# Performance work log

Hardware: AMD Instinct MI355X
Metric: run time of the kernel (lower is better)

## Reference

```python
import jax, jax.numpy as jnp
import numpy as np

B, S, D_MODEL, D_K, D_V = 8, 2048, 1024, 64, 64
NEG = -1e9


def setup_inputs() -> dict:
    key = jax.random.key(0)
    ks = jax.random.split(key, 12)
    inv = 1.0 / np.sqrt(D_MODEL)
    return {
        "q": jax.random.normal(ks[0], (B, S, D_MODEL), jnp.float32),
        "k": jax.random.normal(ks[1], (B, S, D_MODEL), jnp.float32),
        "v": jax.random.normal(ks[2], (B, S, D_MODEL), jnp.float32),
        "mask": jax.random.randint(ks[3], (1, S, S), 0, 2, jnp.int32),
        # Linear weights stored as [in, out] so y = x @ W + b
        "Wq": jax.random.normal(ks[4], (D_MODEL, D_K), jnp.float32) * inv,
        "bq": jnp.zeros((D_K,), jnp.float32),
        "Wk": jax.random.normal(ks[5], (D_MODEL, D_K), jnp.float32) * inv,
        "bk": jnp.zeros((D_K,), jnp.float32),
        "Wv": jax.random.normal(ks[6], (D_MODEL, D_V), jnp.float32) * inv,
        "bv": jnp.zeros((D_V,), jnp.float32),
        "Wo": jax.random.normal(ks[7], (D_V, D_MODEL), jnp.float32) * (1.0 / np.sqrt(D_V)),
        "bo": jnp.zeros((D_MODEL,), jnp.float32),
    }


def reference(q, k, v, mask, Wq, bq, Wk, bk, Wv, bv, Wo, bo):
    # single-head projections: [b, s, d_model] -> [b, s, d_k/d_v]
    qp = q @ Wq + bq
    kp = k @ Wk + bk
    vp = v @ Wv + bv
    # UNSCALED dot-product scores (original has no 1/sqrt(d_k)): [b, s, s]
    scores = jnp.einsum("bqd,bkd->bqk", qp, kp)
    scores = jnp.where(mask == 0, jnp.float32(NEG), scores)
    attn = jax.nn.softmax(scores, axis=-1)  # dropout p=0.0 -> identity
    out = jnp.einsum("bqk,bkv->bqv", attn, vp)
    return out @ Wo + bo
```

## Files before the change

kernel.cpp:

```cpp
#include <hip/hip_runtime.h>
#include <hip/hip_bf16.h>

typedef __bf16 bf16_t;
typedef __attribute__((ext_vector_type(8))) __bf16 bf16x8;
typedef __attribute__((ext_vector_type(4))) float f32x4;

#define MFMA16(a, b, c) __builtin_amdgcn_mfma_f32_16x16x32_bf16((a), (b), (c), 0, 0, 0)

#define NB 8
#define SS 2048
#define DM 1024
#define DK 64
#define NROW (NB * SS)
#define NSPLIT 4
#define SPLEN (SS / NSPLIT)

typedef __attribute__((address_space(1))) const unsigned int ga_u32;
typedef __attribute__((address_space(3))) unsigned int ls_u32;
#define GLOAD16(g, l) \
  __builtin_amdgcn_global_load_lds((ga_u32*)(g), (ls_u32*)(l), 16, 0, 0)

union U16x8 { unsigned short u[8]; uint4 q; };
union U16x4 { unsigned short u[4]; ushort4 v; };

__device__ inline void split_hl(float x, unsigned short& h, unsigned short& l) {
  bf16_t hb = (bf16_t)x;
  bf16_t lb = (bf16_t)(x - (float)hb);
  h = *(unsigned short*)&hb;
  l = *(unsigned short*)&lb;
}

__global__ __launch_bounds__(256) void maskpack_kernel(
    const int* __restrict__ mask, unsigned int* __restrict__ mbits) {
  int idx = blockIdx.x * 256 + threadIdx.x;
  int q = idx >> 6, w = idx & 63;
  const int4* src = (const int4*)(mask + (q << 11) + (w << 5));
  unsigned int bits = 0u;
#pragma unroll
  for (int i = 0; i < 8; ++i) {
    int4 t = src[i];
    bits |= (t.x != 0 ? 1u : 0u) << (i * 4 + 0);
    bits |= (t.y != 0 ? 1u : 0u) << (i * 4 + 1);
    bits |= (t.z != 0 ? 1u : 0u) << (i * 4 + 2);
    bits |= (t.w != 0 ? 1u : 0u) << (i * 4 + 3);
  }
  mbits[idx] = bits;
}

__global__ __launch_bounds__(256) void wprep_kernel(
    const float* __restrict__ Wq, const float* __restrict__ Wk,
    const float* __restrict__ Wv, char* __restrict__ wimg) {
  int which = blockIdx.x >> 6;
  const float* W = which == 0 ? Wq : (which == 1 ? Wk : Wv);
  char* img = wimg + (size_t)which * 16 * 16384;
  int e = (blockIdx.x & 63) * 256 + threadIdx.x;
  int k = e >> 4, n0 = (e & 15) << 2;
  float4 f = *(const float4*)(W + k * 64 + n0);
  float fv[4] = {f.x, f.y, f.z, f.w};
  char* base = img + (k >> 6) * 16384;
  int kk = k & 63;
#pragma unroll
  for (int u = 0; u < 4; ++u) {
    int n = n0 + u;
    unsigned short h, l;
    split_hl(fv[u], h, l);
    int byte = n * 128 + ((2 * kk) ^ ((n & 7) << 4));
    *(unsigned short*)(base + byte) = h;
    *(unsigned short*)(base + 8192 + byte) = l;
  }
}

__global__ __launch_bounds__(256) void proj3_kernel(
    const float* __restrict__ qx, const float* __restrict__ kx,
    const float* __restrict__ vx, const char* __restrict__ wimg,
    const float* __restrict__ bq, const float* __restrict__ bk,
    const float* __restrict__ bv, bf16_t* __restrict__ qhi,
    bf16_t* __restrict__ qlo, char* __restrict__ kimg,
    char* __restrict__ vimg) {
  __shared__ __align__(16) char smem[32768];
  char* xbuf = smem;
  char* wbuf = smem + 16384;
  const int mode = blockIdx.y;
  const float* X = mode == 0 ? qx : (mode == 1 ? kx : vx);
  const float* bias = mode == 0 ? bq : (mode == 1 ? bk : bv);
  const int tid = threadIdx.x;
  const int lane = tid & 63;
  const int wv = tid >> 6;
  const int lr = lane & 15;
  const int g = lane >> 4;
  const int rbase = blockIdx.x * 64;
  const int xr = tid >> 2;
  const int kg = (tid & 3) << 4;
  const int row_local = wv * 16 + lr;
  const int swa = (row_local & 7) << 4;
  const int swx = (xr & 7) << 4;

  f32x4 acc[4] = {};
  const char* wsrc0 = wimg + (size_t)mode * 16 * 16384;

  for (int ch = 0; ch < 16; ++ch) {
    __syncthreads();
    const char* wsrc = wsrc0 + ch * 16384;
#pragma unroll
    for (int u = 0; u < 4; ++u)
      GLOAD16(wsrc + u * 4096 + tid * 16, wbuf + u * 4096 + tid * 16);
    {
      const float4* xp =
          (const float4*)(X + (size_t)(rbase + xr) * DM + ch * 64 + kg);
      float4 a = xp[0], b4 = xp[1], c4 = xp[2], d4 = xp[3];
      float xv[16] = {a.x,  a.y,  a.z,  a.w,  b4.x, b4.y, b4.z, b4.w,
                      c4.x, c4.y, c4.z, c4.w, d4.x, d4.y, d4.z, d4.w};
      U16x8 hq[2], lq[2];
#pragma unroll
      for (int i = 0; i < 16; ++i)
        split_hl(xv[i], hq[i >> 3].u[i & 7], lq[i >> 3].u[i & 7]);
      char* xh = xbuf + xr * 128;
      int b0 = 2 * kg;
      *(uint4*)(xh + ((b0) ^ swx)) = hq[0].q;
      *(uint4*)(xh + ((b0 + 16) ^ swx)) = hq[1].q;
      *(uint4*)(xh + 8192 + ((b0) ^ swx)) = lq[0].q;
      *(uint4*)(xh + 8192 + ((b0 + 16) ^ swx)) = lq[1].q;
    }
    asm volatile("s_waitcnt vmcnt(0)\n" ::: "memory");
    __syncthreads();
#pragma unroll
    for (int ks = 0; ks < 2; ++ks) {
      int co = ks * 64 + g * 16;
      bf16x8 ah = *(const bf16x8*)(xbuf + row_local * 128 + (co ^ swa));
      bf16x8 al = *(const bf16x8*)(xbuf + 8192 + row_local * 128 + (co ^ swa));
#pragma unroll
      for (int c = 0; c < 4; ++c) {
        int n = c * 16 + lr;
        int swb = (n & 7) << 4;
        bf16x8 bh = *(const bf16x8*)(wbuf + n * 128 + (co ^ swb));
        bf16x8 bl = *(const bf16x8*)(wbuf + 8192 + n * 128 + (co ^ swb));
        acc[c] = MFMA16(ah, bl, acc[c]);
        acc[c] = MFMA16(al, bh, acc[c]);
        acc[c] = MFMA16(ah, bh, acc[c]);
      }
    }
  }
  __syncthreads();
  float* sacc = (float*)smem;
#pragma unroll
  for (int c = 0; c < 4; ++c)
#pragma unroll
    for (int j = 0; j < 4; ++j)
      sacc[(wv * 16 + g * 4 + j) * 69 + c * 16 + lr] = acc[c][j];
  __syncthreads();

  const int b = rbase >> 11;
  const int t = (rbase & (SS - 1)) >> 6;
  if (mode == 0) {
    int r = tid & 63, cg = tid >> 6;
    int row = rbase + r;
    U16x8 h0, h1, l0, l1;
#pragma unroll
    for (int i = 0; i < 16; ++i) {
      float v = sacc[r * 69 + cg * 16 + i] + bias[cg * 16 + i];
      if (i < 8) split_hl(v, h0.u[i & 7], l0.u[i & 7]);
      else       split_hl(v, h1.u[i & 7], l1.u[i & 7]);
    }
    *(uint4*)((char*)qhi + (size_t)row * 128 + cg * 32) = h0.q;
    *(uint4*)((char*)qhi + (size_t)row * 128 + cg * 32 + 16) = h1.q;
    *(uint4*)((char*)qlo + (size_t)row * 128 + cg * 32) = l0.q;
    *(uint4*)((char*)qlo + (size_t)row * 128 + cg * 32 + 16) = l1.q;
  } else if (mode == 1) {
    int r = tid & 63, cg = tid >> 6;
    char* base = kimg + (((size_t)(b * 32 + t)) << 14);
    int sw = (r & 7) << 4;
#pragma unroll
    for (int m = 0; m < 4; ++m) {
      U16x4 hv, lv;
#pragma unroll
      for (int u = 0; u < 4; ++u) {
        int col = cg * 16 + m * 4 + u;
        float v = sacc[r * 69 + col] + bias[col];
        split_hl(v, hv.u[u], lv.u[u]);
      }
      int off = (cg * 32 + m * 8) ^ sw;
      *(ushort4*)(base + r * 128 + off) = hv.v;
      *(ushort4*)(base + 8192 + r * 128 + off) = lv.v;
    }
  } else {
    int d = tid & 63, rg = tid >> 6;
    char* base = vimg + (((size_t)(b * 32 + t)) << 14);
    int sw = (d & 7) << 4;
    float bv = bias[d];
#pragma unroll
    for (int m = 0; m < 4; ++m) {
      U16x4 hv, lv;
#pragma unroll
      for (int u = 0; u < 4; ++u) {
        int r = rg * 16 + m * 4 + u;
        float v = sacc[r * 69 + d] + bv;
        split_hl(v, hv.u[u], lv.u[u]);
      }
      int off = (rg * 32 + m * 8) ^ sw;
      *(ushort4*)(base + d * 128 + off) = hv.v;
      *(ushort4*)(base + 8192 + d * 128 + off) = lv.v;
    }
  }
}

__global__ __launch_bounds__(256) void attn_kernel(
    const bf16_t* __restrict__ qhi, const bf16_t* __restrict__ qlo,
    const char* __restrict__ kimg, const char* __restrict__ vimg,
    const unsigned int* __restrict__ mbits, float* __restrict__ part_acc,
    float* __restrict__ part_m, float* __restrict__ part_l) {
  __shared__ __align__(16) char kbuf[16384];
  __shared__ __align__(16) char vbuf[16384];
  __shared__ __align__(16) char plds_all[4][2048];
  const int tid = threadIdx.x;
  const int lane = tid & 63;
  const int wv = tid >> 6;
  const int lr = lane & 15;
  const int g = lane >> 4;
  char* plds = &plds_all[wv][0];
  const int qrow0 = (blockIdx.x * 4 + wv) * 16;
  const int split = blockIdx.y;
  const int kv0 = split * SPLEN;
  const int b = qrow0 >> 11;
  const int sq0 = (qrow0 & (SS - 1)) + g * 4;

  const bf16_t* qh = qhi + (qrow0 + lr) * DK + g * 8;
  const bf16_t* ql = qlo + (qrow0 + lr) * DK + g * 8;
  bf16x8 qh0 = *(const bf16x8*)qh;
  bf16x8 qh1 = *(const bf16x8*)(qh + 32);
  bf16x8 ql0 = *(const bf16x8*)ql;
  bf16x8 ql1 = *(const bf16x8*)(ql + 32);

  float m[4], lsum[4];
  f32x4 acc[4] = {};
#pragma unroll
  for (int j = 0; j < 4; ++j) { m[j] = -3.0e38f; lsum[j] = 0.f; }

  for (int it = 0; it < SPLEN / 64; ++it) {
    const int tglob = (kv0 >> 6) + it;
    const char* ksrc = kimg + (((size_t)(b * 32 + tglob)) << 14);
    const char* vsrc = vimg + (((size_t)(b * 32 + tglob)) << 14);
#pragma unroll
    for (int u = 0; u < 4; ++u) {
      GLOAD16(ksrc + tid * 16 + u * 4096, kbuf + tid * 16 + u * 4096);
      GLOAD16(vsrc + tid * 16 + u * 4096, vbuf + tid * 16 + u * 4096);
    }
    asm volatile("s_waitcnt vmcnt(0)\n" ::: "memory");
    __syncthreads();
    f32x4 sac[4];
#pragma unroll
    for (int t = 0; t < 4; ++t) {
      int rk = t * 16 + lr;
      int sw = (rk & 7) << 4;
      bf16x8 kh0 = *(const bf16x8*)(kbuf + rk * 128 + ((g * 16) ^ sw));
      bf16x8 kh1 = *(const bf16x8*)(kbuf + rk * 128 + ((64 + g * 16) ^ sw));
      bf16x8 kl0 = *(const bf16x8*)(kbuf + 8192 + rk * 128 + ((g * 16) ^ sw));
      bf16x8 kl1 =
          *(const bf16x8*)(kbuf + 8192 + rk * 128 + ((64 + g * 16) ^ sw));
      f32x4 s = {};
      s = MFMA16(qh0, kl0, s);
      s = MFMA16(qh1, kl1, s);
      s = MFMA16(ql0, kh0, s);
      s = MFMA16(ql1, kh1, s);
      s = MFMA16(qh0, kh0, s);
      s = MFMA16(qh1, kh1, s);
      sac[t] = s;
    }
    const int wbase = (kv0 >> 5) + it * 2;
    uint2 m2[4];
#pragma unroll
    for (int j = 0; j < 4; ++j)
      m2[j] = *(const uint2*)(mbits + (sq0 + j) * 64 + wbase);
#pragma unroll
    for (int t = 0; t < 4; ++t)
#pragma unroll
      for (int j = 0; j < 4; ++j) {
        unsigned w = (t & 2) ? m2[j].y : m2[j].x;
        if (!((w >> ((t & 1) * 16 + lr)) & 1u)) sac[t][j] = -1e9f;
      }
#pragma unroll
    for (int j = 0; j < 4; ++j) {
      float v = sac[0][j];
#pragma unroll
      for (int t = 1; t < 4; ++t) v = fmaxf(v, sac[t][j]);
      v = fmaxf(v, __shfl_xor(v, 1, 64));
      v = fmaxf(v, __shfl_xor(v, 2, 64));
      v = fmaxf(v, __shfl_xor(v, 4, 64));
      v = fmaxf(v, __shfl_xor(v, 8, 64));
      float mn = fmaxf(m[j], v);
      float sc = __expf(m[j] - mn);
      m[j] = mn;
      lsum[j] *= sc;
#pragma unroll
      for (int c = 0; c < 4; ++c) acc[c][j] *= sc;
    }
    float ps[4] = {0.f, 0.f, 0.f, 0.f};
#pragma unroll
    for (int t = 0; t < 4; ++t)
#pragma unroll
      for (int j = 0; j < 4; ++j) {
        float p = __expf(sac[t][j] - m[j]);
        bf16_t pb = (bf16_t)p;
        ps[j] += (float)pb;
        int row = g * 4 + j;
        int byte = row * 128 + (((t * 16 + lr) * 2) ^ ((row & 7) << 4));
        *(bf16_t*)(plds + byte) = pb;
      }
#pragma unroll
    for (int j = 0; j < 4; ++j) {
      float s_ = ps[j];
      s_ += __shfl_xor(s_, 1, 64);
      s_ += __shfl_xor(s_, 2, 64);
      s_ += __shfl_xor(s_, 4, 64);
      s_ += __shfl_xor(s_, 8, 64);
      lsum[j] += s_;
    }
    asm volatile("s_waitcnt lgkmcnt(0)\n" ::: "memory");
#pragma unroll
    for (int kt = 0; kt < 2; ++kt) {
      int pbyte = lr * 128 + ((kt * 64 + g * 16) ^ ((lr & 7) << 4));
      bf16x8 pa = *(const bf16x8*)(plds + pbyte);
#pragma unroll
      for (int c = 0; c < 4; ++c) {
        int n = c * 16 + lr;
        int swv = (n & 7) << 4;
        bf16x8 vfh = *(const bf16x8*)(vbuf + n * 128 + ((kt * 64 + g * 16) ^ swv));
        bf16x8 vfl =
            *(const bf16x8*)(vbuf + 8192 + n * 128 + ((kt * 64 + g * 16) ^ swv));
        acc[c] = MFMA16(pa, vfh, acc[c]);
        acc[c] = MFMA16(pa, vfl, acc[c]);
      }
    }
    __syncthreads();
  }
#pragma unroll
  for (int c = 0; c < 4; ++c)
#pragma unroll
    for (int j = 0; j < 4; ++j)
      part_acc[((size_t)split * NROW + qrow0 + g * 4 + j) * DK + c * 16 + lr] =
          acc[c][j];
  if (lr == 0) {
#pragma unroll
    for (int j = 0; j < 4; ++j) {
      part_m[split * NROW + qrow0 + g * 4 + j] = m[j];
      part_l[split * NROW + qrow0 + g * 4 + j] = lsum[j];
    }
  }
}

__global__ __launch_bounds__(256) void combine_kernel(
    const float* __restrict__ pacc, const float* __restrict__ pm,
    const float* __restrict__ pl, float* __restrict__ attn_f) {
  int idx = blockIdx.x * 256 + threadIdx.x;
  int row = idx >> 6;
  float m0 = pm[row], m1 = pm[NROW + row];
  float m2 = pm[2 * NROW + row], m3 = pm[3 * NROW + row];
  float M = fmaxf(fmaxf(m0, m1), fmaxf(m2, m3));
  float w0 = __expf(m0 - M), w1 = __expf(m1 - M);
  float w2 = __expf(m2 - M), w3 = __expf(m3 - M);
  float l = w0 * pl[row] + w1 * pl[NROW + row] + w2 * pl[2 * NROW + row] +
            w3 * pl[3 * NROW + row];
  float a = w0 * pacc[idx] + w1 * pacc[(size_t)NROW * DK + idx] +
            w2 * pacc[2 * (size_t)NROW * DK + idx] +
            w3 * pacc[3 * (size_t)NROW * DK + idx];
  attn_f[idx] = a / l;
}

__global__ __launch_bounds__(256) void oproj_kernel(
    const float* __restrict__ attn, const float* __restrict__ Wo,
    const float* __restrict__ bo, float* __restrict__ out) {
  __shared__ __align__(16) bf16_t wt[256 * 64];
  const int tid = threadIdx.x;
  const int lane = tid & 63;
  const int wv = tid >> 6;
  const int lr = lane & 15;
  const int g = lane >> 4;
  const int rbase = blockIdx.x * 64 + wv * 16;
  const int c0 = blockIdx.y * 256;
  {
    const int k = tid >> 2;
    const int n0 = (tid & 3) << 6;
    const float4* src = (const float4*)(Wo + k * DM + c0 + n0);
#pragma unroll
    for (int i = 0; i < 16; ++i) {
      float4 f = src[i];
      float fv[4] = {f.x, f.y, f.z, f.w};
#pragma unroll
      for (int u = 0; u < 4; ++u) {
        int n = n0 + i * 4 + u;
        int byte = (n << 7) + (k << 1);
        byte ^= (n & 7) << 4;
        *(bf16_t*)((char*)wt + byte) = (bf16_t)fv[u];
      }
    }
  }
  __syncthreads();
  const float* ab = attn + (rbase + lr) * DK + g * 8;
  float4 x0 = *(const float4*)ab;
  float4 x1 = *(const float4*)(ab + 4);
  float4 y0 = *(const float4*)(ab + 32);
  float4 y1 = *(const float4*)(ab + 36);
  float xv[8] = {x0.x, x0.y, x0.z, x0.w, x1.x, x1.y, x1.z, x1.w};
  float yv[8] = {y0.x, y0.y, y0.z, y0.w, y1.x, y1.y, y1.z, y1.w};
  bf16x8 ah0, al0, ah1, al1;
#pragma unroll
  for (int i = 0; i < 8; ++i) {
    ah0[i] = (bf16_t)xv[i];
    al0[i] = (bf16_t)(xv[i] - (float)ah0[i]);
    ah1[i] = (bf16_t)yv[i];
    al1[i] = (bf16_t)(yv[i] - (float)ah1[i]);
  }
  f32x4 acc[16] = {};
#pragma unroll
  for (int c = 0; c < 16; ++c) {
    int n = c * 16 + lr;
    int byte0 = (n << 7) + ((g * 8) << 1);
    byte0 ^= (n & 7) << 4;
    int byte1 = (n << 7) + ((32 + g * 8) << 1);
    byte1 ^= (n & 7) << 4;
    bf16x8 b0 = *(const bf16x8*)((const char*)wt + byte0);
    bf16x8 b1 = *(const bf16x8*)((const char*)wt + byte1);
    acc[c] = MFMA16(ah0, b0, acc[c]);
    acc[c] = MFMA16(al0, b0, acc[c]);
    acc[c] = MFMA16(ah1, b1, acc[c]);
    acc[c] = MFMA16(al1, b1, acc[c]);
  }
#pragma unroll
  for (int c = 0; c < 16; ++c) {
    float bv = bo[c0 + c * 16 + lr];
#pragma unroll
    for (int j = 0; j < 4; ++j)
      out[(rbase + g * 4 + j) * DM + c0 + c * 16 + lr] = acc[c][j] + bv;
  }
}

extern "C" void kernel_launch(void* const* d_in, const int* in_sizes, int n_in,
                              void* d_out, int out_size, void* d_ws,
                              size_t ws_size, hipStream_t stream) {
  const float* q = (const float*)d_in[0];
  const float* k = (const float*)d_in[1];
  const float* v = (const float*)d_in[2];
  const int* mask = (const int*)d_in[3];
  const float* Wq = (const float*)d_in[4];
  const float* bq = (const float*)d_in[5];
  const float* Wk = (const float*)d_in[6];
  const float* bk = (const float*)d_in[7];
  const float* Wv = (const float*)d_in[8];
  const float* bv = (const float*)d_in[9];
  const float* Wo = (const float*)d_in[10];
  const float* bo = (const float*)d_in[11];
  float* out = (float*)d_out;

  bf16_t* qhi = (bf16_t*)d_ws;
  bf16_t* qlo = qhi + (size_t)NROW * DK;
  char* kimg = (char*)(qlo + (size_t)NROW * DK);
  char* vimg = kimg + ((size_t)NB * 32 << 14);
  char* wimg = vimg + ((size_t)NB * 32 << 14);
  float* part_acc = (float*)(wimg + (size_t)3 * 16 * 16384);
  float* part_m = part_acc + (size_t)NSPLIT * NROW * DK;
  float* part_l = part_m + (size_t)NSPLIT * NROW;
  float* attn_f = part_l + (size_t)NSPLIT * NROW;
  unsigned int* mbits = (unsigned int*)(attn_f + (size_t)NROW * DK);

  maskpack_kernel<<<dim3(SS * (SS / 32) / 256), dim3(256), 0, stream>>>(mask,
                                                                        mbits);
  wprep_kernel<<<dim3(192), dim3(256), 0, stream>>>(Wq, Wk, Wv, wimg);
  proj3_kernel<<<dim3(NROW / 64, 3), dim3(256), 0, stream>>>(
      q, k, v, wimg, bq, bk, bv, qhi, qlo, kimg, vimg);
  attn_kernel<<<dim3(NROW / 64, NSPLIT), dim3(256), 0, stream>>>(
      qhi, qlo, kimg, vimg, mbits, part_acc, part_m, part_l);
  combine_kernel<<<dim3(NROW * DK / 256), dim3(256), 0, stream>>>(
      part_acc, part_m, part_l, attn_f);
  oproj_kernel<<<dim3(NROW / 64, DM / 256), dim3(256), 0, stream>>>(attn_f, Wo,
                                                                    bo, out);
}
```

Measured before the change: 142.3 us.

## Double-buffer weight tiles and prefetch X registers in projection kernel

Reworks the projection kernel's K-loop into a software pipeline. Weight chunks are staged into two alternating LDS buffers via global_load_lds, and the X input for two chunks ahead is prefetched into registers, using explicit vmcnt/lgkmcnt waits and barriers. The aim is to overlap global memory latency with the MFMA compute that the previous loop serialized. It increases LDS use from 32KB to 48KB, which can lower occupancy, and the hand-counted waitcnts are fragile.

```diff
diff --git a/kernel.cpp b/kernel.cpp
--- a/kernel.cpp
+++ b/kernel.cpp
@@ -77,9 +77,8 @@
     const float* __restrict__ bv, bf16_t* __restrict__ qhi,
     bf16_t* __restrict__ qlo, char* __restrict__ kimg,
     char* __restrict__ vimg) {
-  __shared__ __align__(16) char smem[32768];
+  __shared__ __align__(16) char smem[49152];
   char* xbuf = smem;
-  char* wbuf = smem + 16384;
   const int mode = blockIdx.y;
   const float* X = mode == 0 ? qx : (mode == 1 ? kx : vx);
   const float* bias = mode == 0 ? bq : (mode == 1 ? bk : bv);
@@ -98,31 +97,33 @@
   f32x4 acc[4] = {};
   const char* wsrc0 = wimg + (size_t)mode * 16 * 16384;
 
-  for (int ch = 0; ch < 16; ++ch) {
-    __syncthreads();
+  float4 xa, xb, xc, xd;
+  auto issueX = [&](int ch) {
+    const float4* xp =
+        (const float4*)(X + (size_t)(rbase + xr) * DM + ch * 64 + kg);
+    xa = xp[0]; xb = xp[1]; xc = xp[2]; xd = xp[3];
+  };
+  auto writeX = [&]() {
+    float xv[16] = {xa.x, xa.y, xa.z, xa.w, xb.x, xb.y, xb.z, xb.w,
+                    xc.x, xc.y, xc.z, xc.w, xd.x, xd.y, xd.z, xd.w};
+    U16x8 hq[2], lq[2];
+#pragma unroll
+    for (int i = 0; i < 16; ++i)
+      split_hl(xv[i], hq[i >> 3].u[i & 7], lq[i >> 3].u[i & 7]);
+    char* xh = xbuf + xr * 128;
+    int b0 = 2 * kg;
+    *(uint4*)(xh + (b0 ^ swx)) = hq[0].q;
+    *(uint4*)(xh + ((b0 + 16) ^ swx)) = hq[1].q;
+    *(uint4*)(xh + 8192 + (b0 ^ swx)) = lq[0].q;
+    *(uint4*)(xh + 8192 + ((b0 + 16) ^ swx)) = lq[1].q;
+  };
+  auto stageW = [&](int ch, char* dst) {
     const char* wsrc = wsrc0 + ch * 16384;
 #pragma unroll
     for (int u = 0; u < 4; ++u)
-      GLOAD16(wsrc + u * 4096 + tid * 16, wbuf + u * 4096 + tid * 16);
-    {
-      const float4* xp =
-          (const float4*)(X + (size_t)(rbase + xr) * DM + ch * 64 + kg);
-      float4 a = xp[0], b4 = xp[1], c4 = xp[2], d4 = xp[3];
-      float xv[16] = {a.x,  a.y,  a.z,  a.w,  b4.x, b4.y, b4.z, b4.w,
-                      c4.x, c4.y, c4.z, c4.w, d4.x, d4.y, d4.z, d4.w};
-      U16x8 hq[2], lq[2];
-#pragma unroll
-      for (int i = 0; i < 16; ++i)
-        split_hl(xv[i], hq[i >> 3].u[i & 7], lq[i >> 3].u[i & 7]);
-      char* xh = xbuf + xr * 128;
-      int b0 = 2 * kg;
-      *(uint4*)(xh + ((b0) ^ swx)) = hq[0].q;
-      *(uint4*)(xh + ((b0 + 16) ^ swx)) = hq[1].q;
-      *(uint4*)(xh + 8192 + ((b0) ^ swx)) = lq[0].q;
-      *(uint4*)(xh + 8192 + ((b0 + 16) ^ swx)) = lq[1].q;
-    }
-    asm volatile("s_waitcnt vmcnt(0)\n" ::: "memory");
-    __syncthreads();
+      GLOAD16(wsrc + u * 4096 + tid * 16, dst + u * 4096 + tid * 16);
+  };
+  auto compute = [&](const char* wb) {
 #pragma unroll
     for (int ks = 0; ks < 2; ++ks) {
       int co = ks * 64 + g * 16;
@@ -132,12 +133,43 @@
       for (int c = 0; c < 4; ++c) {
         int n = c * 16 + lr;
         int swb = (n & 7) << 4;
-        bf16x8 bh = *(const bf16x8*)(wbuf + n * 128 + (co ^ swb));
-        bf16x8 bl = *(const bf16x8*)(wbuf + 8192 + n * 128 + (co ^ swb));
+        bf16x8 bh = *(const bf16x8*)(wb + n * 128 + (co ^ swb));
+        bf16x8 bl = *(const bf16x8*)(wb + 8192 + n * 128 + (co ^ swb));
         acc[c] = MFMA16(ah, bl, acc[c]);
         acc[c] = MFMA16(al, bh, acc[c]);
         acc[c] = MFMA16(ah, bh, acc[c]);
       }
+    }
+  };
+
+  issueX(0);
+  stageW(0, smem + 16384);
+  writeX();
+  issueX(1);
+  asm volatile("s_waitcnt vmcnt(4)" ::: "memory");
+  asm volatile("s_waitcnt lgkmcnt(0)" ::: "memory");
+  __builtin_amdgcn_s_barrier();
+  __builtin_amdgcn_sched_barrier(0);
+
+  for (int ch = 0; ch < 16; ++ch) {
+    char* wc = (ch & 1) ? smem + 32768 : smem + 16384;
+    char* wn = (ch & 1) ? smem + 16384 : smem + 32768;
+    if (ch < 15) stageW(ch + 1, wn);
+    compute(wc);
+    if (ch < 15) {
+      __builtin_amdgcn_sched_barrier(0);
+      __builtin_amdgcn_s_barrier();
+      __builtin_amdgcn_sched_barrier(0);
+      writeX();
+      if (ch < 14) {
+        issueX(ch + 2);
+        asm volatile("s_waitcnt vmcnt(4)" ::: "memory");
+      } else {
+        asm volatile("s_waitcnt vmcnt(0)" ::: "memory");
+      }
+      asm volatile("s_waitcnt lgkmcnt(0)" ::: "memory");
+      __builtin_amdgcn_s_barrier();
+      __builtin_amdgcn_sched_barrier(0);
     }
   }
   __syncthreads();
```

New measurement: 140.6 us (median of 3 runs). Within noise of the previous version (-1.2%).

## Restructure QKV projection: 32-row tiles, async fp32 X staging to LDS

Applied to the files above, without the earlier changes.

The projection kernel now processes 32 rows per block with a 2x2 wave tiling. Raw fp32 X rows are staged into LDS with async global-to-LDS loads in 256-column chunks. The hi/lo bf16 split is done per wave when the fragments are read, instead of through register loads and a split before the LDS store. The grid doubles and the output epilogues write 16-byte vectors. The intent is to make X loads asynchronous and raise parallelism. The cost is more LDS per block (about 49 KB), which may limit occupancy, and split work that is repeated across the wn waves.

```diff
diff --git a/kernel.cpp b/kernel.cpp
--- a/kernel.cpp
+++ b/kernel.cpp
@@ -77,129 +77,136 @@
     const float* __restrict__ bv, bf16_t* __restrict__ qhi,
     bf16_t* __restrict__ qlo, char* __restrict__ kimg,
     char* __restrict__ vimg) {
-  __shared__ __align__(16) char smem[32768];
+  __shared__ __align__(16) char smem[49664];
   char* xbuf = smem;
-  char* wbuf = smem + 16384;
+  char* wbuf = smem + 33280;
   const int mode = blockIdx.y;
   const float* X = mode == 0 ? qx : (mode == 1 ? kx : vx);
   const float* bias = mode == 0 ? bq : (mode == 1 ? bk : bv);
+  const char* Xb = (const char*)X;
   const int tid = threadIdx.x;
   const int lane = tid & 63;
   const int wv = tid >> 6;
   const int lr = lane & 15;
   const int g = lane >> 4;
-  const int rbase = blockIdx.x * 64;
-  const int xr = tid >> 2;
-  const int kg = (tid & 3) << 4;
-  const int row_local = wv * 16 + lr;
-  const int swa = (row_local & 7) << 4;
-  const int swx = (xr & 7) << 4;
-
-  f32x4 acc[4] = {};
+  const int wm = wv & 1;
+  const int wn = wv >> 1;
+  const int rbase = blockIdx.x * 32;
   const char* wsrc0 = wimg + (size_t)mode * 16 * 16384;
 
-  for (int ch = 0; ch < 16; ++ch) {
-    __syncthreads();
-    const char* wsrc = wsrc0 + ch * 16384;
-#pragma unroll
-    for (int u = 0; u < 4; ++u)
-      GLOAD16(wsrc + u * 4096 + tid * 16, wbuf + u * 4096 + tid * 16);
+  f32x4 acc[2] = {};
+
+  auto stageX = [&](int sc) {
+#pragma unroll
+    for (int j = 0; j < 8; ++j) {
+      int u = wv * 8 + j;
+      GLOAD16(Xb + (size_t)(rbase + u) * 4096 + sc * 1024 + lane * 16,
+              xbuf + u * 1040 + lane * 16);
+    }
+  };
+  auto stageW = [&](int idx) {
+    const char* wsrc = wsrc0 + idx * 16384;
+#pragma unroll
+    for (int v = 0; v < 4; ++v)
+      GLOAD16(wsrc + v * 4096 + tid * 16, wbuf + v * 4096 + tid * 16);
+  };
+
+  stageX(0);
+  stageW(0);
+  asm volatile("s_waitcnt vmcnt(0)" ::: "memory");
+  __builtin_amdgcn_s_barrier();
+  __builtin_amdgcn_sched_barrier(0);
+
+  for (int idx = 0; idx < 16; ++idx) {
     {
-      const float4* xp =
-          (const float4*)(X + (size_t)(rbase + xr) * DM + ch * 64 + kg);
-      float4 a = xp[0], b4 = xp[1], c4 = xp[2], d4 = xp[3];
-      float xv[16] = {a.x,  a.y,  a.z,  a.w,  b4.x, b4.y, b4.z, b4.w,
-                      c4.x, c4.y, c4.z, c4.w, d4.x, d4.y, d4.z, d4.w};
-      U16x8 hq[2], lq[2];
-#pragma unroll
-      for (int i = 0; i < 16; ++i)
-        split_hl(xv[i], hq[i >> 3].u[i & 7], lq[i >> 3].u[i & 7]);
-      char* xh = xbuf + xr * 128;
-      int b0 = 2 * kg;
-      *(uint4*)(xh + ((b0) ^ swx)) = hq[0].q;
-      *(uint4*)(xh + ((b0 + 16) ^ swx)) = hq[1].q;
-      *(uint4*)(xh + 8192 + ((b0) ^ swx)) = lq[0].q;
-      *(uint4*)(xh + 8192 + ((b0 + 16) ^ swx)) = lq[1].q;
-    }
-    asm volatile("s_waitcnt vmcnt(0)\n" ::: "memory");
-    __syncthreads();
-#pragma unroll
-    for (int ks = 0; ks < 2; ++ks) {
-      int co = ks * 64 + g * 16;
-      bf16x8 ah = *(const bf16x8*)(xbuf + row_local * 128 + (co ^ swa));
-      bf16x8 al = *(const bf16x8*)(xbuf + 8192 + row_local * 128 + (co ^ swa));
-#pragma unroll
-      for (int c = 0; c < 4; ++c) {
-        int n = c * 16 + lr;
-        int swb = (n & 7) << 4;
-        bf16x8 bh = *(const bf16x8*)(wbuf + n * 128 + (co ^ swb));
-        bf16x8 bl = *(const bf16x8*)(wbuf + 8192 + n * 128 + (co ^ swb));
-        acc[c] = MFMA16(ah, bl, acc[c]);
-        acc[c] = MFMA16(al, bh, acc[c]);
-        acc[c] = MFMA16(ah, bh, acc[c]);
+      const int sub = idx & 3;
+      const char* xrow = xbuf + (wm * 16 + lr) * 1040 + sub * 256;
+#pragma unroll
+      for (int ks = 0; ks < 2; ++ks) {
+        float4 f0 = *(const float4*)(xrow + ks * 128 + g * 32);
+        float4 f1 = *(const float4*)(xrow + ks * 128 + g * 32 + 16);
+        float xv[8] = {f0.x, f0.y, f0.z, f0.w, f1.x, f1.y, f1.z, f1.w};
+        bf16x8 ah, al;
+#pragma unroll
+        for (int i = 0; i < 8; ++i) {
+          unsigned short h, l;
+          split_hl(xv[i], h, l);
+          ((unsigned short*)&ah)[i] = h;
+          ((unsigned short*)&al)[i] = l;
+        }
+#pragma unroll
+        for (int c = 0; c < 2; ++c) {
+          int n = wn * 32 + c * 16 + lr;
+          int swb = (n & 7) << 4;
+          int co = ks * 64 + g * 16;
+          bf16x8 bh = *(const bf16x8*)(wbuf + n * 128 + (co ^ swb));
+          bf16x8 bl = *(const bf16x8*)(wbuf + 8192 + n * 128 + (co ^ swb));
+          acc[c] = MFMA16(ah, bl, acc[c]);
+          acc[c] = MFMA16(al, bh, acc[c]);
+          acc[c] = MFMA16(ah, bh, acc[c]);
+        }
       }
     }
-  }
+    __builtin_amdgcn_sched_barrier(0);
+    __builtin_amdgcn_s_barrier();
+    if (idx < 15) {
+      if ((idx & 3) == 3) stageX((idx >> 2) + 1);
+      stageW(idx + 1);
+      asm volatile("s_waitcnt vmcnt(0)" ::: "memory");
+      __builtin_amdgcn_s_barrier();
+      __builtin_amdgcn_sched_barrier(0);
+    }
+  }
+
   __syncthreads();
   float* sacc = (float*)smem;
 #pragma unroll
-  for (int c = 0; c < 4; ++c)
+  for (int c = 0; c < 2; ++c)
 #pragma unroll
     for (int j = 0; j < 4; ++j)
-      sacc[(wv * 16 + g * 4 + j) * 69 + c * 16 + lr] = acc[c][j];
+      sacc[(wm * 16 + g * 4 + j) * 69 + wn * 32 + c * 16 + lr] = acc[c][j];
   __syncthreads();
 
   const int b = rbase >> 11;
   const int t = (rbase & (SS - 1)) >> 6;
+  const int rt0 = rbase & 63;
   if (mode == 0) {
-    int r = tid & 63, cg = tid >> 6;
+    int r = tid & 31, cg = tid >> 5;
     int row = rbase + r;
-    U16x8 h0, h1, l0, l1;
-#pragma unroll
-    for (int i = 0; i < 16; ++i) {
-      float v = sacc[r * 69 + cg * 16 + i] + bias[cg * 16 + i];
-      if (i < 8) split_hl(v, h0.u[i & 7], l0.u[i & 7]);
-      else       split_hl(v, h1.u[i & 7], l1.u[i & 7]);
-    }
-    *(uint4*)((char*)qhi + (size_t)row * 128 + cg * 32) = h0.q;
-    *(uint4*)((char*)qhi + (size_t)row * 128 + cg * 32 + 16) = h1.q;
-    *(uint4*)((char*)qlo + (size_t)row * 128 + cg * 32) = l0.q;
-    *(uint4*)((char*)qlo + (size_t)row * 128 + cg * 32 + 16) = l1.q;
+    U16x8 h, l;
+#pragma unroll
+    for (int i = 0; i < 8; ++i) {
+      float v = sacc[r * 69 + cg * 8 + i] + bias[cg * 8 + i];
+      split_hl(v, h.u[i], l.u[i]);
+    }
+    *(uint4*)((char*)qhi + (size_t)row * 128 + cg * 16) = h.q;
+    *(uint4*)((char*)qlo + (size_t)row * 128 + cg * 16) = l.q;
   } else if (mode == 1) {
-    int r = tid & 63, cg = tid >> 6;
+    int r = tid & 31, cg = tid >> 5;
+    int rr = rt0 + r;
     char* base = kimg + (((size_t)(b * 32 + t)) << 14);
-    int sw = (r & 7) << 4;
-#pragma unroll
-    for (int m = 0; m < 4; ++m) {
-      U16x4 hv, lv;
-#pragma unroll
-      for (int u = 0; u < 4; ++u) {
-        int col = cg * 16 + m * 4 + u;
-        float v = sacc[r * 69 + col] + bias[col];
-        split_hl(v, hv.u[u], lv.u[u]);
-      }
-      int off = (cg * 32 + m * 8) ^ sw;
-      *(ushort4*)(base + r * 128 + off) = hv.v;
-      *(ushort4*)(base + 8192 + r * 128 + off) = lv.v;
-    }
+    int off = rr * 128 + ((cg * 16) ^ ((rr & 7) << 4));
+    U16x8 h, l;
+#pragma unroll
+    for (int i = 0; i < 8; ++i) {
+      float v = sacc[r * 69 + cg * 8 + i] + bias[cg * 8 + i];
+      split_hl(v, h.u[i], l.u[i]);
+    }
+    *(uint4*)(base + off) = h.q;
+    *(uint4*)(base + 8192 + off) = l.q;
   } else {
     int d = tid & 63, rg = tid >> 6;
     char* base = vimg + (((size_t)(b * 32 + t)) << 14);
-    int sw = (d & 7) << 4;
     float bv = bias[d];
-#pragma unroll
-    for (int m = 0; m < 4; ++m) {
-      U16x4 hv, lv;
-#pragma unroll
-      for (int u = 0; u < 4; ++u) {
-        int r = rg * 16 + m * 4 + u;
-        float v = sacc[r * 69 + d] + bv;
-        split_hl(v, hv.u[u], lv.u[u]);
-      }
-      int off = (rg * 32 + m * 8) ^ sw;
-      *(ushort4*)(base + d * 128 + off) = hv.v;
-      *(ushort4*)(base + 8192 + d * 128 + off) = lv.v;
-    }
+    U16x8 h, l;
+#pragma unroll
+    for (int i = 0; i < 8; ++i) {
+      float v = sacc[(rg * 8 + i) * 69 + d] + bv;
+      split_hl(v, h.u[i], l.u[i]);
+    }
+    int off = d * 128 + (((rt0 + rg * 8) * 2) ^ ((d & 7) << 4));
+    *(uint4*)(base + off) = h.q;
+    *(uint4*)(base + 8192 + off) = l.q;
   }
 }
 
@@ -464,7 +471,7 @@
   maskpack_kernel<<<dim3(SS * (SS / 32) / 256), dim3(256), 0, stream>>>(mask,
                                                                         mbits);
   wprep_kernel<<<dim3(192), dim3(256), 0, stream>>>(Wq, Wk, Wv, wimg);
-  proj3_kernel<<<dim3(NROW / 64, 3), dim3(256), 0, stream>>>(
+  proj3_kernel<<<dim3(NROW / 32, 3), dim3(256), 0, stream>>>(
       q, k, v, wimg, bq, bk, bv, qhi, qlo, kimg, vimg);
   attn_kernel<<<dim3(NROW / 64, NSPLIT), dim3(256), 0, stream>>>(
       qhi, qlo, kimg, vimg, mbits, part_acc, part_m, part_l);
```

After: 147.7 us. 3.8% more time.
